# Kernel tuning notes

Measured on AMD Instinct MI355X. Metric: run time of the kernel, lower is better.

## Reference

```python
import jax, jax.numpy as jnp
import numpy as np

B, S, D, H = 2, 2048, 512, 8
DH = D // H  # d_head = 64


def sparsemax(z):
    """Sparsemax over last axis: Euclidean projection of z onto the simplex."""
    n = z.shape[-1]
    z_sorted = -jnp.sort(-z, axis=-1)                      # descending
    z_cumsum = jnp.cumsum(z_sorted, axis=-1)
    r = jnp.arange(1, n + 1, dtype=z.dtype)
    support = r * z_sorted > z_cumsum - 1.0                # 1 + k*z_(k) > cumsum_k
    k = jnp.sum(support, axis=-1, keepdims=True)           # support size (int)
    tau = (jnp.take_along_axis(z_cumsum, k - 1, axis=-1) - 1.0) / k.astype(z.dtype)
    return jnp.maximum(z - tau, 0.0)


def setup_inputs() -> dict:
    key = jax.random.key(0)
    ks = jax.random.split(key, 6)
    scale_in = 1.0 / np.sqrt(D)
    qk_scale = 1.0 / np.sqrt(DH)  # module folds 1/sqrt(d_head) into W_q at init
    x = jax.random.normal(ks[0], (B, S, D), dtype=jnp.float32)
    Wq = jax.random.normal(ks[1], (D, D), dtype=jnp.float32) * (scale_in * qk_scale)
    Wk = jax.random.normal(ks[2], (D, D), dtype=jnp.float32) * scale_in
    Wv = jax.random.normal(ks[3], (D, DH), dtype=jnp.float32) * scale_in
    Wout = jax.random.normal(ks[4], (D, D), dtype=jnp.float32) * scale_in
    return {
        "x": x,
        "Wq": Wq, "bq": jnp.zeros((D,), jnp.float32),
        "Wk": Wk, "bk": jnp.zeros((D,), jnp.float32),
        "Wv": Wv, "bv": jnp.zeros((DH,), jnp.float32),
        "Wout": Wout, "bout": jnp.zeros((D,), jnp.float32),
    }


def reference(x, Wq, bq, Wk, bk, Wv, bv, Wout, bout):
    b, s, d = x.shape
    q = (x @ Wq + bq).reshape(b, s, H, DH).transpose(0, 2, 1, 3)  # [B,H,S,dh]
    k = (x @ Wk + bk).reshape(b, s, H, DH).transpose(0, 2, 1, 3)  # [B,H,S,dh]
    v = x @ Wv + bv                                                # shared V [B,S,dh]
    # No 1/sqrt(d_head) here: the module bakes it into W_q at init.
    logits = jnp.einsum("bhqd,bhkd->bhqk", q, k)                   # [B,H,S,S]
    probs = sparsemax(logits)                                      # row-sparse simplex
    heads = jnp.einsum("bhqk,bkd->bhqd", probs, v)                 # shared V across heads
    x_out = heads.transpose(0, 2, 1, 3).reshape(b, s, d)
    x_out = x_out @ Wout + bout                                    # W_out (n_heads > 1)
    avg_attention = probs.mean(axis=1)                             # [B,S,S]
    return (x_out, avg_attention)
```

## Files before the change

kernel.cpp:

```cpp
#include <hip/hip_runtime.h>
#include <cstddef>
#include <cstdint>

#define TS 2048
#define TD 512
#define TH 8
#define TDH 64
#define CAP 256

typedef float f32x4 __attribute__((ext_vector_type(4)));
typedef short short8v __attribute__((ext_vector_type(8)));
typedef _Float16 half4v __attribute__((ext_vector_type(4)));
typedef _Float16 half8v __attribute__((ext_vector_type(8)));

__device__ __forceinline__ unsigned short f2bf(float f) {
  unsigned u = __builtin_bit_cast(unsigned, f);
  u += 0x7fff + ((u >> 16) & 1);
  return (unsigned short)(u >> 16);
}

__global__ __launch_bounds__(256) void proj_gemm(
    const float* __restrict__ x,
    const float* __restrict__ Wq, const float* __restrict__ bq,
    const float* __restrict__ Wk, const float* __restrict__ bk,
    const float* __restrict__ Wv, const float* __restrict__ bv,
    short* __restrict__ Qh, short* __restrict__ Kh, float* __restrict__ Vb)
{
  __shared__ short As[64][40];
  __shared__ short Bs[64][40];

  const int by = blockIdx.y;
  const float* W; const float* bias; int N; int col0; int outsel;
  if (by < 8)       { W = Wq; bias = bq; N = TD;  col0 = by * 64;       outsel = 0; }
  else if (by < 16) { W = Wk; bias = bk; N = TD;  col0 = (by - 8) * 64; outsel = 1; }
  else              { W = Wv; bias = bv; N = TDH; col0 = 0;             outsel = 2; }

  const int tid  = threadIdx.x;
  const int w    = tid >> 6;
  const int lane = tid & 63;
  const int g    = lane >> 4;
  const int lc16 = lane & 15;
  const int wm   = w >> 1;
  const int wn   = w & 1;
  const int row0 = blockIdx.x * 64;

  const int ar = tid >> 2;
  const int ak = (tid & 3) << 3;
  const int wk = tid >> 3;
  const int wn8 = (tid & 7) << 3;

  f32x4 acc[2][2];
#pragma unroll
  for (int i = 0; i < 2; ++i)
#pragma unroll
    for (int j = 0; j < 2; ++j) acc[i][j] = (f32x4){0.f, 0.f, 0.f, 0.f};

  for (int kt = 0; kt < TD; kt += 32) {
    {
      const float* ap = x + (size_t)(row0 + ar) * TD + kt + ak;
      float4 f0 = *(const float4*)ap;
      float4 f1 = *(const float4*)(ap + 4);
      short8v v;
      v[0] = (short)f2bf(f0.x); v[1] = (short)f2bf(f0.y);
      v[2] = (short)f2bf(f0.z); v[3] = (short)f2bf(f0.w);
      v[4] = (short)f2bf(f1.x); v[5] = (short)f2bf(f1.y);
      v[6] = (short)f2bf(f1.z); v[7] = (short)f2bf(f1.w);
      *(short8v*)&As[ar][ak] = v;
    }
    {
      const float* wp = W + (size_t)(kt + wk) * N + col0 + wn8;
      float4 f0 = *(const float4*)wp;
      float4 f1 = *(const float4*)(wp + 4);
      Bs[wn8 + 0][wk] = (short)f2bf(f0.x);
      Bs[wn8 + 1][wk] = (short)f2bf(f0.y);
      Bs[wn8 + 2][wk] = (short)f2bf(f0.z);
      Bs[wn8 + 3][wk] = (short)f2bf(f0.w);
      Bs[wn8 + 4][wk] = (short)f2bf(f1.x);
      Bs[wn8 + 5][wk] = (short)f2bf(f1.y);
      Bs[wn8 + 6][wk] = (short)f2bf(f1.z);
      Bs[wn8 + 7][wk] = (short)f2bf(f1.w);
    }
    __syncthreads();

    short8v a0 = *(const short8v*)&As[wm * 32 + lc16][g * 8];
    short8v a1 = *(const short8v*)&As[wm * 32 + 16 + lc16][g * 8];
    short8v b0 = *(const short8v*)&Bs[wn * 32 + lc16][g * 8];
    short8v b1 = *(const short8v*)&Bs[wn * 32 + 16 + lc16][g * 8];
    acc[0][0] = __builtin_amdgcn_mfma_f32_16x16x32_bf16(a0, b0, acc[0][0], 0, 0, 0);
    acc[0][1] = __builtin_amdgcn_mfma_f32_16x16x32_bf16(a0, b1, acc[0][1], 0, 0, 0);
    acc[1][0] = __builtin_amdgcn_mfma_f32_16x16x32_bf16(a1, b0, acc[1][0], 0, 0, 0);
    acc[1][1] = __builtin_amdgcn_mfma_f32_16x16x32_bf16(a1, b1, acc[1][1], 0, 0, 0);
    __syncthreads();
  }

  short* Obf = (outsel == 0) ? Qh : Kh;
#pragma unroll
  for (int ni = 0; ni < 2; ++ni) {
    const int ocol = col0 + wn * 32 + ni * 16 + lc16;
    if (ocol >= N) continue;
    const float bb = bias[ocol];
#pragma unroll
    for (int mi = 0; mi < 2; ++mi)
#pragma unroll
      for (int r = 0; r < 4; ++r) {
        const int orow = row0 + wm * 32 + mi * 16 + g * 4 + r;
        const float val = acc[mi][ni][r] + bb;
        if (outsel == 2) {
          Vb[(size_t)orow * TDH + ocol] = val;
        } else {
          const int bI = orow >> 11, s = orow & 2047;
          const int hI = ocol >> 6, dh = ocol & 63;
          Obf[(((size_t)(bI * TH + hI) * TS + s) * TDH) + dh] = (short)f2bf(val);
        }
      }
  }
}

__global__ __launch_bounds__(256) void gemm_out(
    const short* __restrict__ A, const float* __restrict__ W,
    const float* __restrict__ bias, float* __restrict__ Cf, int N, int Kd)
{
  __shared__ short As[64][40];
  __shared__ short Bs[64][40];

  const int tid  = threadIdx.x;
  const int w    = tid >> 6;
  const int lane = tid & 63;
  const int g    = lane >> 4;
  const int lc16 = lane & 15;
  const int wm   = w >> 1;
  const int wn   = w & 1;
  const int row0 = blockIdx.x * 64;
  const int col0 = blockIdx.y * 64;

  const int ar = tid >> 2;
  const int ak = (tid & 3) << 3;
  const int wk = tid >> 3;
  const int wn8 = (tid & 7) << 3;

  f32x4 acc[2][2];
#pragma unroll
  for (int i = 0; i < 2; ++i)
#pragma unroll
    for (int j = 0; j < 2; ++j) acc[i][j] = (f32x4){0.f, 0.f, 0.f, 0.f};

  for (int kt = 0; kt < Kd; kt += 32) {
    {
      short8v v = *(const short8v*)(A + (size_t)(row0 + ar) * Kd + kt + ak);
      *(short8v*)&As[ar][ak] = v;
    }
    {
      const float* wp = W + (size_t)(kt + wk) * N + col0 + wn8;
      float4 f0 = *(const float4*)wp;
      float4 f1 = *(const float4*)(wp + 4);
      Bs[wn8 + 0][wk] = (short)f2bf(f0.x);
      Bs[wn8 + 1][wk] = (short)f2bf(f0.y);
      Bs[wn8 + 2][wk] = (short)f2bf(f0.z);
      Bs[wn8 + 3][wk] = (short)f2bf(f0.w);
      Bs[wn8 + 4][wk] = (short)f2bf(f1.x);
      Bs[wn8 + 5][wk] = (short)f2bf(f1.y);
      Bs[wn8 + 6][wk] = (short)f2bf(f1.z);
      Bs[wn8 + 7][wk] = (short)f2bf(f1.w);
    }
    __syncthreads();

    short8v a0 = *(const short8v*)&As[wm * 32 + lc16][g * 8];
    short8v a1 = *(const short8v*)&As[wm * 32 + 16 + lc16][g * 8];
    short8v b0 = *(const short8v*)&Bs[wn * 32 + lc16][g * 8];
    short8v b1 = *(const short8v*)&Bs[wn * 32 + 16 + lc16][g * 8];
    acc[0][0] = __builtin_amdgcn_mfma_f32_16x16x32_bf16(a0, b0, acc[0][0], 0, 0, 0);
    acc[0][1] = __builtin_amdgcn_mfma_f32_16x16x32_bf16(a0, b1, acc[0][1], 0, 0, 0);
    acc[1][0] = __builtin_amdgcn_mfma_f32_16x16x32_bf16(a1, b0, acc[1][0], 0, 0, 0);
    acc[1][1] = __builtin_amdgcn_mfma_f32_16x16x32_bf16(a1, b1, acc[1][1], 0, 0, 0);
    __syncthreads();
  }

#pragma unroll
  for (int ni = 0; ni < 2; ++ni) {
    const int ocol = col0 + wn * 32 + ni * 16 + lc16;
    const float bb = bias[ocol];
#pragma unroll
    for (int mi = 0; mi < 2; ++mi)
#pragma unroll
      for (int r = 0; r < 4; ++r) {
        const int orow = row0 + wm * 32 + mi * 16 + g * 4 + r;
        Cf[(size_t)orow * N + ocol] = acc[mi][ni][r] + bb;
      }
  }
}

__global__ __launch_bounds__(256) void zgemm(
    const short* __restrict__ Qh, const short* __restrict__ Kh,
    _Float16* __restrict__ Zh, int bsel, int q0s, int qc)
{
  const int tid  = threadIdx.x;
  const int w    = tid >> 6;
  const int lane = tid & 63;
  const int g    = lane >> 4;
  const int lc16 = lane & 15;
  const int h    = blockIdx.z;
  const int pair = bsel * TH + h;
  const int jb   = blockIdx.x * 256 + w * 64;
  const int qlb  = blockIdx.y * 64;
  const int qb   = q0s + qlb;

  const short* Qp = Qh + (size_t)pair * TS * TDH;
  const short* Kp = Kh + (size_t)pair * TS * TDH;

  short8v bq[4][2];
#pragma unroll
  for (int ct = 0; ct < 4; ++ct) {
    const short* qp = Qp + (size_t)(qb + ct * 16 + lc16) * TDH + g * 8;
    bq[ct][0] = *(const short8v*)qp;
    bq[ct][1] = *(const short8v*)(qp + 32);
  }

  f32x4 acc[4][4];
#pragma unroll
  for (int rt = 0; rt < 4; ++rt)
#pragma unroll
    for (int ct = 0; ct < 4; ++ct) acc[rt][ct] = (f32x4){0.f, 0.f, 0.f, 0.f};

#pragma unroll
  for (int rt = 0; rt < 4; ++rt) {
    const short* kp = Kp + (size_t)(jb + rt * 16 + lc16) * TDH + g * 8;
    short8v ak0 = *(const short8v*)kp;
    short8v ak1 = *(const short8v*)(kp + 32);
#pragma unroll
    for (int ct = 0; ct < 4; ++ct) {
      acc[rt][ct] = __builtin_amdgcn_mfma_f32_16x16x32_bf16(ak0, bq[ct][0], acc[rt][ct], 0, 0, 0);
      acc[rt][ct] = __builtin_amdgcn_mfma_f32_16x16x32_bf16(ak1, bq[ct][1], acc[rt][ct], 0, 0, 0);
    }
  }

#pragma unroll
  for (int rt = 0; rt < 4; ++rt)
#pragma unroll
    for (int ct = 0; ct < 4; ++ct) {
      half4v o = {(_Float16)acc[rt][ct][0], (_Float16)acc[rt][ct][1],
                  (_Float16)acc[rt][ct][2], (_Float16)acc[rt][ct][3]};
      *(half4v*)&Zh[((size_t)h * qc + qlb + ct * 16 + lc16) * TS + jb + rt * 16 + g * 4] = o;
    }
}

__global__ __launch_bounds__(512) void spv(
    const _Float16* __restrict__ Zh, const float* __restrict__ V,
    short* __restrict__ heads, float* __restrict__ avg,
    int bsel, int q0s, int qc)
{
  __shared__ float avgS[TS];
  __shared__ unsigned short idxW[TH][CAP];
  __shared__ float pW[TH][CAP];
  __shared__ int cntW[TH];

  const int tid  = threadIdx.x;
  const int h    = tid >> 6;
  const int lane = tid & 63;
  const int ql   = blockIdx.x;
  const int q    = q0s + ql;
  const int row  = bsel * TS + q;
  const float* Vb = V + (size_t)bsel * TS * TDH;

  *(f32x4*)&avgS[tid << 2] = (f32x4){0.f, 0.f, 0.f, 0.f};
  if (lane == 0) cntW[h] = 0;
  __syncthreads();

  float za[4][8];
  const _Float16* zp = Zh + ((size_t)h * qc + ql) * TS;
#pragma unroll
  for (int k = 0; k < 4; ++k) {
    half8v v = *(const half8v*)(zp + (k << 9) + (lane << 3));
#pragma unroll
    for (int c = 0; c < 8; ++c) za[k][c] = (float)v[c];
  }

  float m = za[0][0];
#pragma unroll
  for (int k = 0; k < 4; ++k)
#pragma unroll
    for (int c = 0; c < 8; ++c) m = fmaxf(m, za[k][c]);
#pragma unroll
  for (int s = 1; s < 64; s <<= 1) m = fmaxf(m, __shfl_xor(m, s));
  const float tau0 = m - 1.0f;

  float c0 = -1e30f, c1 = -1e30f, c2 = -1e30f, c3 = -1e30f;
  int j0 = 0, j1 = 0, j2 = 0, j3 = 0, nc = 0;
#pragma unroll
  for (int k = 0; k < 4; ++k)
#pragma unroll
    for (int c = 0; c < 8; ++c) {
      const float v = za[k][c];
      if (v > tau0) {
        c3 = c2; j3 = j2; c2 = c1; j2 = j1; c1 = c0; j1 = j0;
        c0 = v; j0 = (k << 9) + (lane << 3) + c; ++nc;
      }
    }
  const bool over = (__ballot(nc > 4) != 0ull);

  float tau = tau0;
  int prevc = -1;
  if (!over) {
    for (int it = 0; it < 64; ++it) {
      float s = 0.f, c = 0.f;
      if (c0 > tau) { s += c0; c += 1.f; }
      if (c1 > tau) { s += c1; c += 1.f; }
      if (c2 > tau) { s += c2; c += 1.f; }
      if (c3 > tau) { s += c3; c += 1.f; }
#pragma unroll
      for (int sh = 1; sh < 64; sh <<= 1) {
        s += __shfl_xor(s, sh);
        c += __shfl_xor(c, sh);
      }
      tau = (s - 1.f) / c;
      const int ci = (int)c;
      if (ci == prevc) break;
      prevc = ci;
    }
  } else {
    for (int it = 0; it < 64; ++it) {
      float s = 0.f, c = 0.f;
#pragma unroll
      for (int k = 0; k < 4; ++k)
#pragma unroll
        for (int cc = 0; cc < 8; ++cc) {
          const float v = za[k][cc];
          if (v > tau) { s += v; c += 1.f; }
        }
#pragma unroll
      for (int sh = 1; sh < 64; sh <<= 1) {
        s += __shfl_xor(s, sh);
        c += __shfl_xor(c, sh);
      }
      tau = (s - 1.f) / c;
      const int ci = (int)c;
      if (ci == prevc) break;
      prevc = ci;
    }
  }

  if (!over) {
    {
      const float p = c0 - tau;
      if (p > 0.f) {
        atomicAdd(&avgS[j0], p);
        const int pos = atomicAdd(&cntW[h], 1);
        if (pos < CAP) { idxW[h][pos] = (unsigned short)j0; pW[h][pos] = p; }
      }
    }
    {
      const float p = c1 - tau;
      if (p > 0.f) {
        atomicAdd(&avgS[j1], p);
        const int pos = atomicAdd(&cntW[h], 1);
        if (pos < CAP) { idxW[h][pos] = (unsigned short)j1; pW[h][pos] = p; }
      }
    }
    {
      const float p = c2 - tau;
      if (p > 0.f) {
        atomicAdd(&avgS[j2], p);
        const int pos = atomicAdd(&cntW[h], 1);
        if (pos < CAP) { idxW[h][pos] = (unsigned short)j2; pW[h][pos] = p; }
      }
    }
    {
      const float p = c3 - tau;
      if (p > 0.f) {
        atomicAdd(&avgS[j3], p);
        const int pos = atomicAdd(&cntW[h], 1);
        if (pos < CAP) { idxW[h][pos] = (unsigned short)j3; pW[h][pos] = p; }
      }
    }
  } else {
#pragma unroll
    for (int k = 0; k < 4; ++k)
#pragma unroll
      for (int cc = 0; cc < 8; ++cc) {
        const float p = za[k][cc] - tau;
        if (p > 0.f) {
          const int j = (k << 9) + (lane << 3) + cc;
          atomicAdd(&avgS[j], p);
          const int pos = atomicAdd(&cntW[h], 1);
          if (pos < CAP) { idxW[h][pos] = (unsigned short)j; pW[h][pos] = p; }
        }
      }
  }

  const int cnt = cntW[h];
  float a = 0.f;
  if (cnt <= CAP) {
    for (int e0 = 0; e0 < cnt; e0 += 8) {
      float pb[8], vb8[8];
#pragma unroll
      for (int u = 0; u < 8; ++u) {
        const int e = e0 + u;
        const int ec = (e < cnt) ? e : 0;
        pb[u] = (e < cnt) ? pW[h][ec] : 0.f;
        vb8[u] = Vb[(size_t)idxW[h][ec] * TDH + lane];
      }
#pragma unroll
      for (int u = 0; u < 8; ++u) a += pb[u] * vb8[u];
    }
  } else {
#pragma unroll
    for (int k = 0; k < 4; ++k)
#pragma unroll
      for (int cc = 0; cc < 8; ++cc) {
        const float p = za[k][cc] - tau;
        unsigned long long mask = __ballot(p > 0.f);
        while (mask) {
          const int src = __ffsll((long long)mask) - 1;
          mask &= mask - 1;
          const float pj = __shfl(p, src);
          const int j = (k << 9) + (src << 3) + cc;
          a += pj * Vb[(size_t)j * TDH + lane];
        }
      }
  }
  heads[(size_t)row * TD + h * TDH + lane] = (short)f2bf(a);

  __syncthreads();
  {
    f32x4 t = *(const f32x4*)&avgS[tid << 2];
    float4 o = {t[0] * 0.125f, t[1] * 0.125f, t[2] * 0.125f, t[3] * 0.125f};
    *(float4*)(avg + (size_t)row * TS + (tid << 2)) = o;
  }
}

extern "C" void kernel_launch(void* const* d_in, const int* in_sizes, int n_in,
                              void* d_out, int out_size, void* d_ws, size_t ws_size,
                              hipStream_t stream) {
  (void)in_sizes; (void)n_in; (void)out_size;

  const float* x    = (const float*)d_in[0];
  const float* Wq   = (const float*)d_in[1];
  const float* bq   = (const float*)d_in[2];
  const float* Wk   = (const float*)d_in[3];
  const float* bk   = (const float*)d_in[4];
  const float* Wv   = (const float*)d_in[5];
  const float* bv   = (const float*)d_in[6];
  const float* Wout = (const float*)d_in[7];
  const float* bout = (const float*)d_in[8];

  float* out   = (float*)d_out;
  float* x_out = out;
  float* avg   = out + 2097152;

  float* ws = (float*)d_ws;
  float* Vb = ws;
  short* Hd = (short*)(ws + 262144);
  short* Qh = (short*)(ws + 1310720);
  short* Kh = (short*)(ws + 2359296);
  _Float16* Zh = (_Float16*)(ws + 3407872);

  const size_t wsFloats = ws_size / 4;
  const size_t base = 3407872;
  int qc = 64;
  for (int cand = 2048; cand >= 64; cand >>= 1) {
    if (base + (size_t)TH * cand * TS / 2 <= wsFloats) { qc = cand; break; }
  }

  const dim3 blk(256);
  const int BS = 2 * TS;

  proj_gemm<<<dim3(BS / 64, 17), blk, 0, stream>>>(x, Wq, bq, Wk, bk, Wv, bv, Qh, Kh, Vb);

  for (int bsel = 0; bsel < 2; ++bsel)
    for (int q0s = 0; q0s < TS; q0s += qc) {
      zgemm<<<dim3(TS / 256, qc / 64, TH), blk, 0, stream>>>(Qh, Kh, Zh, bsel, q0s, qc);
      spv<<<dim3(qc), dim3(512), 0, stream>>>(Zh, Vb, Hd, avg, bsel, q0s, qc);
    }

  gemm_out<<<dim3(BS / 64, TD / 64), blk, 0, stream>>>(Hd, Wout, bout, x_out, TD, TD);
}
```

Before: 164.7 us.

## Batch both sequences per launch, stage Z tile in LDS, preconvert x to bf16

Merges the two batch iterations into single zgemm/spv launches by adding a batch grid dimension, which halves the launch count and raises per-launch parallelism at the cost of a larger Z workspace and possibly a smaller query chunk. The zgemm output tile is transposed through shared memory so global writes of Z become contiguous 16-byte rows. A separate conversion kernel turns x into bf16 once instead of converting it in all 17 projection column blocks, which adds one kernel launch and a workspace buffer.

New measurement: 139.1 us. 1.18x faster.

```diff
diff --git a/kernel.cpp b/kernel.cpp
--- a/kernel.cpp
+++ b/kernel.cpp
@@ -19,8 +19,22 @@
   return (unsigned short)(u >> 16);
 }
 
+__global__ __launch_bounds__(256) void cvt_bf16(
+    const float* __restrict__ x, short* __restrict__ xb)
+{
+  const int i = (blockIdx.x * 256 + threadIdx.x) << 3;
+  float4 f0 = *(const float4*)(x + i);
+  float4 f1 = *(const float4*)(x + i + 4);
+  short8v v;
+  v[0] = (short)f2bf(f0.x); v[1] = (short)f2bf(f0.y);
+  v[2] = (short)f2bf(f0.z); v[3] = (short)f2bf(f0.w);
+  v[4] = (short)f2bf(f1.x); v[5] = (short)f2bf(f1.y);
+  v[6] = (short)f2bf(f1.z); v[7] = (short)f2bf(f1.w);
+  *(short8v*)(xb + i) = v;
+}
+
 __global__ __launch_bounds__(256) void proj_gemm(
-    const float* __restrict__ x,
+    const short* __restrict__ xb,
     const float* __restrict__ Wq, const float* __restrict__ bq,
     const float* __restrict__ Wk, const float* __restrict__ bk,
     const float* __restrict__ Wv, const float* __restrict__ bv,
@@ -57,14 +71,7 @@
 
   for (int kt = 0; kt < TD; kt += 32) {
     {
-      const float* ap = x + (size_t)(row0 + ar) * TD + kt + ak;
-      float4 f0 = *(const float4*)ap;
-      float4 f1 = *(const float4*)(ap + 4);
-      short8v v;
-      v[0] = (short)f2bf(f0.x); v[1] = (short)f2bf(f0.y);
-      v[2] = (short)f2bf(f0.z); v[3] = (short)f2bf(f0.w);
-      v[4] = (short)f2bf(f1.x); v[5] = (short)f2bf(f1.y);
-      v[6] = (short)f2bf(f1.z); v[7] = (short)f2bf(f1.w);
+      short8v v = *(const short8v*)(xb + (size_t)(row0 + ar) * TD + kt + ak);
       *(short8v*)&As[ar][ak] = v;
     }
     {
@@ -191,16 +198,17 @@
 
 __global__ __launch_bounds__(256) void zgemm(
     const short* __restrict__ Qh, const short* __restrict__ Kh,
-    _Float16* __restrict__ Zh, int bsel, int q0s, int qc)
+    _Float16* __restrict__ Zh, int q0s, int qc)
 {
+  __shared__ _Float16 Zt[64][264];
+
   const int tid  = threadIdx.x;
   const int w    = tid >> 6;
   const int lane = tid & 63;
   const int g    = lane >> 4;
   const int lc16 = lane & 15;
-  const int h    = blockIdx.z;
-  const int pair = bsel * TH + h;
-  const int jb   = blockIdx.x * 256 + w * 64;
+  const int pair = blockIdx.z;
+  const int jb0  = blockIdx.x * 256;
   const int qlb  = blockIdx.y * 64;
   const int qb   = q0s + qlb;
 
@@ -223,7 +231,7 @@
 
 #pragma unroll
   for (int rt = 0; rt < 4; ++rt) {
-    const short* kp = Kp + (size_t)(jb + rt * 16 + lc16) * TDH + g * 8;
+    const short* kp = Kp + (size_t)(jb0 + w * 64 + rt * 16 + lc16) * TDH + g * 8;
     short8v ak0 = *(const short8v*)kp;
     short8v ak1 = *(const short8v*)(kp + 32);
 #pragma unroll
@@ -239,14 +247,24 @@
     for (int ct = 0; ct < 4; ++ct) {
       half4v o = {(_Float16)acc[rt][ct][0], (_Float16)acc[rt][ct][1],
                   (_Float16)acc[rt][ct][2], (_Float16)acc[rt][ct][3]};
-      *(half4v*)&Zh[((size_t)h * qc + qlb + ct * 16 + lc16) * TS + jb + rt * 16 + g * 4] = o;
-    }
+      *(half4v*)&Zt[ct * 16 + lc16][w * 64 + rt * 16 + g * 4] = o;
+    }
+  __syncthreads();
+
+  const int rseg = tid >> 5;
+  const int jseg = (tid & 31) << 3;
+#pragma unroll
+  for (int i = 0; i < 8; ++i) {
+    const int r = (i << 3) + rseg;
+    half8v v = *(const half8v*)&Zt[r][jseg];
+    *(half8v*)&Zh[((size_t)pair * qc + qlb + r) * TS + jb0 + jseg] = v;
+  }
 }
 
 __global__ __launch_bounds__(512) void spv(
     const _Float16* __restrict__ Zh, const float* __restrict__ V,
     short* __restrict__ heads, float* __restrict__ avg,
-    int bsel, int q0s, int qc)
+    int q0s, int qc)
 {
   __shared__ float avgS[TS];
   __shared__ unsigned short idxW[TH][CAP];
@@ -257,6 +275,7 @@
   const int h    = tid >> 6;
   const int lane = tid & 63;
   const int ql   = blockIdx.x;
+  const int bsel = blockIdx.y;
   const int q    = q0s + ql;
   const int row  = bsel * TS + q;
   const float* Vb = V + (size_t)bsel * TS * TDH;
@@ -266,7 +285,7 @@
   __syncthreads();
 
   float za[4][8];
-  const _Float16* zp = Zh + ((size_t)h * qc + ql) * TS;
+  const _Float16* zp = Zh + ((size_t)(bsel * TH + h) * qc + ql) * TS;
 #pragma unroll
   for (int k = 0; k < 4; ++k) {
     half8v v = *(const half8v*)(zp + (k << 9) + (lane << 3));
@@ -452,24 +471,25 @@
   short* Qh = (short*)(ws + 1310720);
   short* Kh = (short*)(ws + 2359296);
   _Float16* Zh = (_Float16*)(ws + 3407872);
+  short* xbuf = (short*)(ws + 3407872);
 
   const size_t wsFloats = ws_size / 4;
   const size_t base = 3407872;
   int qc = 64;
   for (int cand = 2048; cand >= 64; cand >>= 1) {
-    if (base + (size_t)TH * cand * TS / 2 <= wsFloats) { qc = cand; break; }
+    if (base + (size_t)16 * cand * 1024 <= wsFloats) { qc = cand; break; }
   }
 
   const dim3 blk(256);
   const int BS = 2 * TS;
 
-  proj_gemm<<<dim3(BS / 64, 17), blk, 0, stream>>>(x, Wq, bq, Wk, bk, Wv, bv, Qh, Kh, Vb);
-
-  for (int bsel = 0; bsel < 2; ++bsel)
-    for (int q0s = 0; q0s < TS; q0s += qc) {
-      zgemm<<<dim3(TS / 256, qc / 64, TH), blk, 0, stream>>>(Qh, Kh, Zh, bsel, q0s, qc);
-      spv<<<dim3(qc), dim3(512), 0, stream>>>(Zh, Vb, Hd, avg, bsel, q0s, qc);
-    }
+  cvt_bf16<<<dim3(BS * TD / (256 * 8)), blk, 0, stream>>>(x, xbuf);
+  proj_gemm<<<dim3(BS / 64, 17), blk, 0, stream>>>(xbuf, Wq, bq, Wk, bk, Wv, bv, Qh, Kh, Vb);
+
+  for (int q0s = 0; q0s < TS; q0s += qc) {
+    zgemm<<<dim3(TS / 256, qc / 64, 16), blk, 0, stream>>>(Qh, Kh, Zh, q0s, qc);
+    spv<<<dim3(qc, 2), dim3(512), 0, stream>>>(Zh, Vb, Hd, avg, q0s, qc);
+  }
 
   gemm_out<<<dim3(BS / 64, TD / 64), blk, 0, stream>>>(Hd, Wout, bout, x_out, TD, TD);
 }
```
